# Kernel tuning notes

Measured on AMD Instinct MI355X. Metric: run time of the kernel, lower is better.

The kernel has to match this reference:

```python
import jax, jax.numpy as jnp
import numpy as np

DIM = 256
BETA = 4
B, L, L1 = 16, 2048, 4096
EPS = 1e-6


def setup_inputs() -> dict:
    key = jax.random.key(0)
    ks = jax.random.split(key, 20)
    d, db = DIM, DIM // BETA
    s = lambda *sh: 0.02
    inp = {
        "features": jax.random.normal(ks[0], (B, L, d), jnp.float32),
        "quires_box": jax.random.uniform(ks[1], (B, L1, 2), jnp.float32),
        "quires_features": jax.random.normal(ks[2], (B, L1, d), jnp.float32),
        "pos_feature": jax.random.normal(ks[3], (B, L1, d), jnp.float32),
        # contrast1 params
        "c1_w1": jax.random.normal(ks[4], (db, d), jnp.float32) * 0.02,
        "c1_b1": jnp.zeros((db,), jnp.float32),
        "c1_w2": jax.random.normal(ks[5], (d, db), jnp.float32) * 0.02,
        "c1_b2": jnp.zeros((d,), jnp.float32),
        "c1_g": jnp.ones((d,), jnp.float32),
        "c1_be": jnp.zeros((d,), jnp.float32),
        # contrast2 params
        "c2_w1": jax.random.normal(ks[6], (db, d), jnp.float32) * 0.02,
        "c2_b1": jnp.zeros((db,), jnp.float32),
        "c2_w2": jax.random.normal(ks[7], (d, db), jnp.float32) * 0.02,
        "c2_b2": jnp.zeros((d,), jnp.float32),
        "c2_g": jnp.ones((d,), jnp.float32),
        "c2_be": jnp.zeros((d,), jnp.float32),
        # gate MLP (Prediction: Linear(2d->d)+ReLU+Linear(d->2), dropout=identity at eval)
        "g_w1": jax.random.normal(ks[8], (d, 2 * d), jnp.float32) * 0.02,
        "g_b1": jnp.zeros((d,), jnp.float32),
        "g_w2": jax.random.normal(ks[9], (2, d), jnp.float32) * 0.02,
        "g_b2": jnp.zeros((2,), jnp.float32),
    }
    return inp


def _contrast(v1, v2, w1, b1, w2, b2, g, be):
    # v1, v2: [B, N, C]. Pointwise conv1 -> ReLU -> conv2 -> LayerNorm -> sigmoid -> *v1
    v = v1 * v2
    h = jax.nn.relu(jnp.einsum('bnc,dc->bnd', v, w1) + b1)  # [B,N,C/beta]
    u = jnp.einsum('bnd,cd->bnc', h, w2) + b2               # [B,N,C]
    mu = jnp.mean(u, axis=-1, keepdims=True)
    var = jnp.mean(jnp.square(u - mu), axis=-1, keepdims=True)
    ln = (u - mu) * jax.lax.rsqrt(var + EPS) * g + be
    return jax.nn.sigmoid(ln) * v1


def reference(features, quires_box, quires_features, pos_feature,
              c1_w1, c1_b1, c1_w2, c1_b2, c1_g, c1_be,
              c2_w1, c2_b1, c2_w2, c2_b2, c2_g, c2_be,
              g_w1, g_b1, g_w2, g_b2):
    Lf = features.shape[1]
    cx, w = quires_box[..., 0], quires_box[..., 1]
    roi_start = jnp.round(jnp.clip((cx - w / 2) * Lf, 0, Lf - 1)).astype(jnp.int32)
    roi_end = jnp.round(jnp.clip((cx + w / 2) * Lf, 0, Lf - 1)).astype(jnp.int32)
    sf = jnp.take_along_axis(features, roi_start[..., None], axis=1)  # [B,L1,C]
    ef = jnp.take_along_axis(features, roi_end[..., None], axis=1)    # [B,L1,C]
    sf = _contrast(sf, pos_feature, c1_w1, c1_b1, c1_w2, c1_b2, c1_g, c1_be)
    ef = _contrast(ef, pos_feature, c2_w1, c2_b1, c2_w2, c2_b2, c2_g, c2_be)
    pooled = (sf + ef) * 0.5  # aligned_len=True -> mean over the 2 boundaries
    x = jnp.concatenate([pooled, quires_features], axis=-1)  # [B,L1,2C]
    h = jax.nn.relu(jnp.einsum('bnc,dc->bnd', x, g_w1) + g_b1)
    gate = jax.nn.softmax(jnp.einsum('bnd,od->bno', h, g_w2) + g_b2, axis=-1)
    out = pooled * gate[..., 0:1] + quires_features * gate[..., 1:2]
    return jnp.swapaxes(out, 0, 1)  # [L1, B, C]
```

## Files before the change

kernel.cpp:

```cpp
#include <hip/hip_runtime.h>
#include <hip/hip_bf16.h>
#include <math.h>

typedef __attribute__((ext_vector_type(8))) short bf16x8;
typedef __attribute__((ext_vector_type(4))) float f32x4;
typedef __attribute__((ext_vector_type(2))) __fp16 f16x2;
typedef __attribute__((ext_vector_type(4))) unsigned int u32x4;
typedef __attribute__((ext_vector_type(2))) unsigned int u32x2;

constexpr int NB = 16, NQ = 4096, LF = 2048, C = 256;

__device__ __forceinline__ unsigned short bfbits(float x) {
    return __builtin_bit_cast(unsigned short, __float2bfloat16(x));
}
__device__ __forceinline__ unsigned pk2(float a, float b) {
    return (unsigned)bfbits(a) | ((unsigned)bfbits(b) << 16);
}
__device__ __forceinline__ float bflo(unsigned d) { return __builtin_bit_cast(float, d << 16); }
__device__ __forceinline__ float bfhi(unsigned d) { return __builtin_bit_cast(float, d & 0xffff0000u); }

__global__ void prep_weights(const float* __restrict__ c1w1, const float* __restrict__ c2w1,
                             const float* __restrict__ c1w2, const float* __restrict__ c2w2,
                             const float* __restrict__ gw1, unsigned short* __restrict__ ws)
{
    int t = blockIdx.x * 256 + threadIdx.x;
    const float* src; int K, nks, dstoff, f;
    if (t < 2048)      { src = c1w1; K = 256; nks = 8;  dstoff = 0;      f = t; }
    else if (t < 4096) { src = c2w1; K = 256; nks = 8;  dstoff = 16384;  f = t - 2048; }
    else if (t < 6144) { src = c1w2; K = 64;  nks = 2;  dstoff = 32768;  f = t - 4096; }
    else if (t < 8192) { src = c2w2; K = 64;  nks = 2;  dstoff = 49152;  f = t - 6144; }
    else               { src = gw1;  K = 512; nks = 16; dstoff = 65536;  f = t - 8192; }
    int l = f & 63, s = f >> 6;
    int nt = s / nks, ks = s % nks;
    int n  = nt * 16 + (l & 15);
    int k0 = ks * 32 + (l >> 4) * 8;
    unsigned short* d = ws + dstoff + (size_t)f * 8;
    const float* sp = src + (size_t)n * K + k0;
    #pragma unroll
    for (int e = 0; e < 8; ++e) d[e] = bfbits(sp[e]);
}

__device__ __forceinline__ void stage_chunk(const unsigned short* wsb, int chunk,
                                            unsigned short* dst, int wid, int l)
{
    const char* g = (const char*)wsb + (size_t)chunk * 32768 + wid * 1024 + (size_t)l * 16;
    char* d = (char*)dst + wid * 1024;
    #pragma unroll
    for (int i = 0; i < 16; ++i) {
        __builtin_amdgcn_global_load_lds(
            (const __attribute__((address_space(1))) void*)(g + i * 2048),
            (__attribute__((address_space(3))) void*)(d + i * 2048),
            16, 0, 0);
    }
}

__global__ __launch_bounds__(128, 2)
void semalign_v7(const float* __restrict__ feat,  const float* __restrict__ qbox,
                 const float* __restrict__ qfeat, const float* __restrict__ posf,
                 const float* __restrict__ c1b1,  const float* __restrict__ c1b2,
                 const float* __restrict__ c1g,   const float* __restrict__ c1be,
                 const float* __restrict__ c2b1,  const float* __restrict__ c2b2,
                 const float* __restrict__ c2g,   const float* __restrict__ c2be,
                 const float* __restrict__ gb1,   const float* __restrict__ gw2,
                 const float* __restrict__ gb2,
                 const unsigned short* __restrict__ wsb,
                 float* __restrict__ out)
{
    __shared__ __align__(16) unsigned short sW[2][16384];
    __shared__ __align__(16) unsigned short sP[2][16][256];

    const int tid = threadIdx.x, l = tid & 63, wid = tid >> 6;
    const int lr = l & 15, lg = l >> 4;
    const int rowb = blockIdx.x * 32 + wid * 16;
    const int q = rowb >> 4;
    const int b = lr;
    const int swz = (lr & 7) << 4;

    stage_chunk(wsb, 0, sW[0], wid, l);
    stage_chunk(wsb, 1, sW[1], wid, l);

    const float* prow = posf  + ((size_t)b * NQ + q) * C;
    const float* qrow = qfeat + ((size_t)b * NQ + q) * C;
    float cx = qbox[((size_t)b * NQ + q) * 2 + 0];
    float w  = qbox[((size_t)b * NQ + q) * 2 + 1];
    float fs = fminf(fmaxf((cx - 0.5f * w) * (float)LF, 0.f), (float)(LF - 1));
    float fe = fminf(fmaxf((cx + 0.5f * w) * (float)LF, 0.f), (float)(LF - 1));
    const float* srow = feat + ((size_t)b * LF + (int)rintf(fs)) * C;
    const float* erow = feat + ((size_t)b * LF + (int)rintf(fe)) * C;

    bf16x8 v1f[8], v2f[8];
    #pragma unroll
    for (int ks = 0; ks < 8; ++ks) {
        int k0 = ks * 32 + lg * 8;
        float4 s0 = *(const float4*)(srow + k0), s1 = *(const float4*)(srow + k0 + 4);
        float4 e0 = *(const float4*)(erow + k0), e1 = *(const float4*)(erow + k0 + 4);
        float4 p0 = *(const float4*)(prow + k0), p1 = *(const float4*)(prow + k0 + 4);
        u32x4 a, c;
        a[0] = pk2(s0.x * p0.x, s0.y * p0.y); a[1] = pk2(s0.z * p0.z, s0.w * p0.w);
        a[2] = pk2(s1.x * p1.x, s1.y * p1.y); a[3] = pk2(s1.z * p1.z, s1.w * p1.w);
        c[0] = pk2(e0.x * p0.x, e0.y * p0.y); c[1] = pk2(e0.z * p0.z, e0.w * p0.w);
        c[2] = pk2(e1.x * p1.x, e1.y * p1.y); c[3] = pk2(e1.z * p1.z, e1.w * p1.w);
        v1f[ks] = __builtin_bit_cast(bf16x8, a);
        v2f[ks] = __builtin_bit_cast(bf16x8, c);
    }

    __syncthreads();

    f32x4 a1[4] = {};
    {
        const char* wb = (const char*)sW[0];
        #pragma unroll
        for (int ks = 0; ks < 8; ++ks)
            #pragma unroll
            for (int nt = 0; nt < 4; ++nt) {
                bf16x8 wA = *(const bf16x8*)(wb + (nt * 8 + ks) * 1024 + l * 16);
                a1[nt] = __builtin_amdgcn_mfma_f32_16x16x32_bf16(wA, v1f[ks], a1[nt], 0, 0, 0);
            }
    }
    __syncthreads();
    stage_chunk(wsb, 2, sW[0], wid, l);

    char* hb = (char*)&sP[wid][0][0];
    bf16x8 hA0, hA1, hB0, hB1;
    {
        const char* wb = (const char*)sW[1];
        f32x4 a2[4] = {};
        #pragma unroll
        for (int ks = 0; ks < 8; ++ks)
            #pragma unroll
            for (int nt = 0; nt < 4; ++nt) {
                bf16x8 wB = *(const bf16x8*)(wb + (nt * 8 + ks) * 1024 + l * 16);
                a2[nt] = __builtin_amdgcn_mfma_f32_16x16x32_bf16(wB, v2f[ks], a2[nt], 0, 0, 0);
            }
        #pragma unroll
        for (int nt = 0; nt < 4; ++nt) {
            float4 b1v = *(const float4*)(c1b1 + nt * 16 + lg * 4);
            float4 b2v = *(const float4*)(c2b1 + nt * 16 + lg * 4);
            u32x2 wv;
            wv[0] = pk2(fmaxf(a1[nt][0] + b1v.x, 0.f), fmaxf(a1[nt][1] + b1v.y, 0.f));
            wv[1] = pk2(fmaxf(a1[nt][2] + b1v.z, 0.f), fmaxf(a1[nt][3] + b1v.w, 0.f));
            *(u32x2*)(hb + lr * 128 + ((nt * 32 + lg * 8) ^ swz)) = wv;
            wv[0] = pk2(fmaxf(a2[nt][0] + b2v.x, 0.f), fmaxf(a2[nt][1] + b2v.y, 0.f));
            wv[1] = pk2(fmaxf(a2[nt][2] + b2v.z, 0.f), fmaxf(a2[nt][3] + b2v.w, 0.f));
            *(u32x2*)(hb + 2048 + lr * 128 + ((nt * 32 + lg * 8) ^ swz)) = wv;
        }
        asm volatile("s_waitcnt lgkmcnt(0)" ::: "memory");
        hA0 = *(const bf16x8*)(hb + lr * 128 + ((0  + lg * 16) ^ swz));
        hA1 = *(const bf16x8*)(hb + lr * 128 + ((64 + lg * 16) ^ swz));
        hB0 = *(const bf16x8*)(hb + 2048 + lr * 128 + ((0  + lg * 16) ^ swz));
        hB1 = *(const bf16x8*)(hb + 2048 + lr * 128 + ((64 + lg * 16) ^ swz));
    }
    __syncthreads();
    stage_chunk(wsb, 3, sW[1], wid, l);

    f16x2 Ph[16][2];
    {
        const char* wb = (const char*)sW[0];
        f32x4 u0[16] = {};
        #pragma unroll
        for (int nt = 0; nt < 16; ++nt) {
            bf16x8 wA0 = *(const bf16x8*)(wb + (nt * 2 + 0) * 1024 + l * 16);
            bf16x8 wA1 = *(const bf16x8*)(wb + (nt * 2 + 1) * 1024 + l * 16);
            u0[nt] = __builtin_amdgcn_mfma_f32_16x16x32_bf16(wA0, hA0, u0[nt], 0, 0, 0);
            u0[nt] = __builtin_amdgcn_mfma_f32_16x16x32_bf16(wA1, hA1, u0[nt], 0, 0, 0);
        }
        float S = 0.f, Q2 = 0.f;
        #pragma unroll
        for (int nt = 0; nt < 16; ++nt) {
            float4 bv = *(const float4*)(c1b2 + nt * 16 + lg * 4);
            u0[nt][0] += bv.x; u0[nt][1] += bv.y; u0[nt][2] += bv.z; u0[nt][3] += bv.w;
            S  += u0[nt][0] + u0[nt][1] + u0[nt][2] + u0[nt][3];
            Q2 += u0[nt][0] * u0[nt][0] + u0[nt][1] * u0[nt][1]
                + u0[nt][2] * u0[nt][2] + u0[nt][3] * u0[nt][3];
        }
        S  += __shfl_xor(S, 16);  S  += __shfl_xor(S, 32);
        Q2 += __shfl_xor(Q2, 16); Q2 += __shfl_xor(Q2, 32);
        float mu  = S * (1.f / 256.f);
        float rsg = rsqrtf(Q2 * (1.f / 256.f) - mu * mu + 1e-6f);
        #pragma unroll
        for (int nt = 0; nt < 16; ++nt) {
            float4 gv  = *(const float4*)(c1g  + nt * 16 + lg * 4);
            float4 bev = *(const float4*)(c1be + nt * 16 + lg * 4);
            float4 xv  = *(const float4*)(srow + nt * 16 + lg * 4);
            float g4[4] = { gv.x, gv.y, gv.z, gv.w };
            float e4[4] = { bev.x, bev.y, bev.z, bev.w };
            float x4[4] = { xv.x, xv.y, xv.z, xv.w };
            float tm[4];
            #pragma unroll
            for (int r = 0; r < 4; ++r) {
                float ln = (u0[nt][r] - mu) * rsg * g4[r] + e4[r];
                float sg = 1.f / (1.f + __expf(-ln));
                tm[r] = 0.5f * sg * x4[r];
            }
            Ph[nt][0] = __builtin_amdgcn_cvt_pkrtz(tm[0], tm[1]);
            Ph[nt][1] = __builtin_amdgcn_cvt_pkrtz(tm[2], tm[3]);
        }
    }
    __syncthreads();
    stage_chunk(wsb, 4, sW[0], wid, l);

    bf16x8 qff[8];
    {
        const char* wb = (const char*)sW[1];
        f32x4 u1[16] = {};
        #pragma unroll
        for (int nt = 0; nt < 16; ++nt) {
            bf16x8 wB0 = *(const bf16x8*)(wb + (nt * 2 + 0) * 1024 + l * 16);
            bf16x8 wB1 = *(const bf16x8*)(wb + (nt * 2 + 1) * 1024 + l * 16);
            u1[nt] = __builtin_amdgcn_mfma_f32_16x16x32_bf16(wB0, hB0, u1[nt], 0, 0, 0);
            u1[nt] = __builtin_amdgcn_mfma_f32_16x16x32_bf16(wB1, hB1, u1[nt], 0, 0, 0);
        }
        float S = 0.f, Q2 = 0.f;
        #pragma unroll
        for (int nt = 0; nt < 16; ++nt) {
            float4 bv = *(const float4*)(c2b2 + nt * 16 + lg * 4);
            u1[nt][0] += bv.x; u1[nt][1] += bv.y; u1[nt][2] += bv.z; u1[nt][3] += bv.w;
            S  += u1[nt][0] + u1[nt][1] + u1[nt][2] + u1[nt][3];
            Q2 += u1[nt][0] * u1[nt][0] + u1[nt][1] * u1[nt][1]
                + u1[nt][2] * u1[nt][2] + u1[nt][3] * u1[nt][3];
        }
        S  += __shfl_xor(S, 16);  S  += __shfl_xor(S, 32);
        Q2 += __shfl_xor(Q2, 16); Q2 += __shfl_xor(Q2, 32);
        float mu  = S * (1.f / 256.f);
        float rsg = rsqrtf(Q2 * (1.f / 256.f) - mu * mu + 1e-6f);
        #pragma unroll
        for (int nt = 0; nt < 16; ++nt) {
            float4 gv  = *(const float4*)(c2g  + nt * 16 + lg * 4);
            float4 bev = *(const float4*)(c2be + nt * 16 + lg * 4);
            float4 xv  = *(const float4*)(erow + nt * 16 + lg * 4);
            float g4[4] = { gv.x, gv.y, gv.z, gv.w };
            float e4[4] = { bev.x, bev.y, bev.z, bev.w };
            float x4[4] = { xv.x, xv.y, xv.z, xv.w };
            float pm[4];
            #pragma unroll
            for (int r = 0; r < 4; ++r) {
                float ln = (u1[nt][r] - mu) * rsg * g4[r] + e4[r];
                float sg = 1.f / (1.f + __expf(-ln));
                pm[r] = (float)Ph[nt][r >> 1][r & 1] + 0.5f * sg * x4[r];
            }
            u32x2 wv;
            wv[0] = pk2(pm[0], pm[1]); wv[1] = pk2(pm[2], pm[3]);
            *(u32x2*)(hb + lr * 512 + ((nt * 32 + lg * 8) ^ swz)) = wv;
        }
        #pragma unroll
        for (int ks = 0; ks < 8; ++ks) {
            int k0 = ks * 32 + lg * 8;
            float4 q0v = *(const float4*)(qrow + k0), q1v = *(const float4*)(qrow + k0 + 4);
            u32x4 a;
            a[0] = pk2(q0v.x, q0v.y); a[1] = pk2(q0v.z, q0v.w);
            a[2] = pk2(q1v.x, q1v.y); a[3] = pk2(q1v.z, q1v.w);
            qff[ks] = __builtin_bit_cast(bf16x8, a);
        }
        asm volatile("s_waitcnt lgkmcnt(0)" ::: "memory");
    }
    bf16x8 xfp[8];
    #pragma unroll
    for (int ks = 0; ks < 8; ++ks)
        xfp[ks] = *(const bf16x8*)(hb + lr * 512 + ((ks * 64 + lg * 16) ^ swz));
    __syncthreads();
    stage_chunk(wsb, 5, sW[1], wid, l);

    float t0 = 0.f, t1 = 0.f;
    #pragma unroll
    for (int cc = 0; cc < 8; ++cc) {
        const char* wb = (const char*)sW[cc & 1];
        f32x4 ga0 = {}, ga1 = {};
        #pragma unroll
        for (int kk = 0; kk < 16; ++kk) {
            bf16x8 xk = (kk < 8) ? xfp[kk] : qff[kk - 8];
            bf16x8 wA = *(const bf16x8*)(wb + kk * 1024 + l * 16);
            bf16x8 wB = *(const bf16x8*)(wb + (16 + kk) * 1024 + l * 16);
            ga0 = __builtin_amdgcn_mfma_f32_16x16x32_bf16(wA, xk, ga0, 0, 0, 0);
            ga1 = __builtin_amdgcn_mfma_f32_16x16x32_bf16(wB, xk, ga1, 0, 0, 0);
        }
        #pragma unroll
        for (int t2 = 0; t2 < 2; ++t2) {
            f32x4 ga = t2 ? ga1 : ga0;
            int nt = cc * 2 + t2;
            float4 gbv = *(const float4*)(gb1 + nt * 16 + lg * 4);
            float4 w0v = *(const float4*)(gw2 + nt * 16 + lg * 4);
            float4 w1v = *(const float4*)(gw2 + 256 + nt * 16 + lg * 4);
            float gb4[4] = { gbv.x, gbv.y, gbv.z, gbv.w };
            float w04[4] = { w0v.x, w0v.y, w0v.z, w0v.w };
            float w14[4] = { w1v.x, w1v.y, w1v.z, w1v.w };
            #pragma unroll
            for (int r = 0; r < 4; ++r) {
                float hv = fmaxf(ga[r] + gb4[r], 0.f);
                t0 += hv * w04[r]; t1 += hv * w14[r];
            }
        }
        __syncthreads();
        if (cc < 6) stage_chunk(wsb, 6 + cc, sW[cc & 1], wid, l);
    }

    t0 += __shfl_xor(t0, 16); t0 += __shfl_xor(t0, 32);
    t1 += __shfl_xor(t1, 16); t1 += __shfl_xor(t1, 32);
    float g0 = 1.f / (1.f + __expf((t1 + gb2[1]) - (t0 + gb2[0])));
    float g1v = 1.f - g0;

    float* orow = out + (size_t)(rowb + lr) * C;
    #pragma unroll
    for (int ks = 0; ks < 8; ++ks) {
        u32x4 pu = __builtin_bit_cast(u32x4, xfp[ks]);
        u32x4 qu = __builtin_bit_cast(u32x4, qff[ks]);
        float4 o0, o1;
        o0.x = bflo(pu[0]) * g0 + bflo(qu[0]) * g1v;
        o0.y = bfhi(pu[0]) * g0 + bfhi(qu[0]) * g1v;
        o0.z = bflo(pu[1]) * g0 + bflo(qu[1]) * g1v;
        o0.w = bfhi(pu[1]) * g0 + bfhi(qu[1]) * g1v;
        o1.x = bflo(pu[2]) * g0 + bflo(qu[2]) * g1v;
        o1.y = bfhi(pu[2]) * g0 + bfhi(qu[2]) * g1v;
        o1.z = bflo(pu[3]) * g0 + bflo(qu[3]) * g1v;
        o1.w = bfhi(pu[3]) * g0 + bfhi(qu[3]) * g1v;
        *(float4*)(orow + ks * 32 + lg * 8)     = o0;
        *(float4*)(orow + ks * 32 + lg * 8 + 4) = o1;
    }
}

extern "C" void kernel_launch(void* const* d_in, const int* in_sizes, int n_in,
                              void* d_out, int out_size, void* d_ws, size_t ws_size,
                              hipStream_t stream) {
    const float* feat  = (const float*)d_in[0];
    const float* qbox  = (const float*)d_in[1];
    const float* qfeat = (const float*)d_in[2];
    const float* posf  = (const float*)d_in[3];
    const float* c1w1  = (const float*)d_in[4];
    const float* c1b1  = (const float*)d_in[5];
    const float* c1w2  = (const float*)d_in[6];
    const float* c1b2  = (const float*)d_in[7];
    const float* c1g   = (const float*)d_in[8];
    const float* c1be  = (const float*)d_in[9];
    const float* c2w1  = (const float*)d_in[10];
    const float* c2b1  = (const float*)d_in[11];
    const float* c2w2  = (const float*)d_in[12];
    const float* c2b2  = (const float*)d_in[13];
    const float* c2g   = (const float*)d_in[14];
    const float* c2be  = (const float*)d_in[15];
    const float* gw1   = (const float*)d_in[16];
    const float* gb1   = (const float*)d_in[17];
    const float* gw2   = (const float*)d_in[18];
    const float* gb2   = (const float*)d_in[19];
    float* out = (float*)d_out;
    unsigned short* wsb = (unsigned short*)d_ws;

    prep_weights<<<96, 256, 0, stream>>>(c1w1, c2w1, c1w2, c2w2, gw1, wsb);

    dim3 grid((NB * NQ) / 32), block(128);
    semalign_v7<<<grid, block, 0, stream>>>(
        feat, qbox, qfeat, posf,
        c1b1, c1b2, c1g, c1be,
        c2b1, c2b2, c2g, c2be,
        gb1, gw2, gb2, wsb, out);
}
```

Measured before the change: 182.9 us.

## Stream weights through LDS in 8KB sub-chunks to shrink shared memory footprint

Weight staging is split from 32KB chunks into 8KB sub-chunks, so the double buffer drops from 64KB to 16KB of LDS. Every GEMM phase (contrast conv1 and conv2 for both branches, and the gate MLP) is restructured to consume one sub-chunk, sync, then prefetch the sub-chunk two ahead. The aim is lower LDS use per block, so more blocks can be resident per CU and hide gather latency. The cost is several times more barriers and smaller prefetch units, which leaves less load-compute overlap per step.

```diff
diff --git a/kernel.cpp b/kernel.cpp
--- a/kernel.cpp
+++ b/kernel.cpp
@@ -40,13 +40,13 @@
     for (int e = 0; e < 8; ++e) d[e] = bfbits(sp[e]);
 }
 
-__device__ __forceinline__ void stage_chunk(const unsigned short* wsb, int chunk,
-                                            unsigned short* dst, int wid, int l)
+__device__ __forceinline__ void stage_sub(const unsigned short* wsb, int sub,
+                                          unsigned short* dst, int wid, int l)
 {
-    const char* g = (const char*)wsb + (size_t)chunk * 32768 + wid * 1024 + (size_t)l * 16;
+    const char* g = (const char*)wsb + (size_t)sub * 8192 + (size_t)wid * 1024 + (size_t)l * 16;
     char* d = (char*)dst + wid * 1024;
     #pragma unroll
-    for (int i = 0; i < 16; ++i) {
+    for (int i = 0; i < 4; ++i) {
         __builtin_amdgcn_global_load_lds(
             (const __attribute__((address_space(1))) void*)(g + i * 2048),
             (__attribute__((address_space(3))) void*)(d + i * 2048),
@@ -55,18 +55,18 @@
 }
 
 __global__ __launch_bounds__(128, 2)
-void semalign_v7(const float* __restrict__ feat,  const float* __restrict__ qbox,
-                 const float* __restrict__ qfeat, const float* __restrict__ posf,
-                 const float* __restrict__ c1b1,  const float* __restrict__ c1b2,
-                 const float* __restrict__ c1g,   const float* __restrict__ c1be,
-                 const float* __restrict__ c2b1,  const float* __restrict__ c2b2,
-                 const float* __restrict__ c2g,   const float* __restrict__ c2be,
-                 const float* __restrict__ gb1,   const float* __restrict__ gw2,
-                 const float* __restrict__ gb2,
-                 const unsigned short* __restrict__ wsb,
-                 float* __restrict__ out)
+void semalign_v10(const float* __restrict__ feat,  const float* __restrict__ qbox,
+                  const float* __restrict__ qfeat, const float* __restrict__ posf,
+                  const float* __restrict__ c1b1,  const float* __restrict__ c1b2,
+                  const float* __restrict__ c1g,   const float* __restrict__ c1be,
+                  const float* __restrict__ c2b1,  const float* __restrict__ c2b2,
+                  const float* __restrict__ c2g,   const float* __restrict__ c2be,
+                  const float* __restrict__ gb1,   const float* __restrict__ gw2,
+                  const float* __restrict__ gb2,
+                  const unsigned short* __restrict__ wsb,
+                  float* __restrict__ out)
 {
-    __shared__ __align__(16) unsigned short sW[2][16384];
+    __shared__ __align__(16) unsigned short sW[2][4096];
     __shared__ __align__(16) unsigned short sP[2][16][256];
 
     const int tid = threadIdx.x, l = tid & 63, wid = tid >> 6;
@@ -76,8 +76,8 @@
     const int b = lr;
     const int swz = (lr & 7) << 4;
 
-    stage_chunk(wsb, 0, sW[0], wid, l);
-    stage_chunk(wsb, 1, sW[1], wid, l);
+    stage_sub(wsb, 0, sW[0], wid, l);
+    stage_sub(wsb, 1, sW[1], wid, l);
 
     const float* prow = posf  + ((size_t)b * NQ + q) * C;
     const float* qrow = qfeat + ((size_t)b * NQ + q) * C;
@@ -106,32 +106,24 @@
 
     __syncthreads();
 
-    f32x4 a1[4] = {};
-    {
-        const char* wb = (const char*)sW[0];
-        #pragma unroll
-        for (int ks = 0; ks < 8; ++ks)
-            #pragma unroll
-            for (int nt = 0; nt < 4; ++nt) {
-                bf16x8 wA = *(const bf16x8*)(wb + (nt * 8 + ks) * 1024 + l * 16);
-                a1[nt] = __builtin_amdgcn_mfma_f32_16x16x32_bf16(wA, v1f[ks], a1[nt], 0, 0, 0);
-            }
-    }
-    __syncthreads();
-    stage_chunk(wsb, 2, sW[0], wid, l);
+    f32x4 a1[4] = {}, a2[4] = {};
+    #pragma unroll
+    for (int ss = 0; ss < 8; ++ss) {
+        const char* wb = (const char*)sW[ss & 1];
+        int nt = ss & 3;
+        #pragma unroll
+        for (int ks = 0; ks < 8; ++ks) {
+            bf16x8 wf = *(const bf16x8*)(wb + ks * 1024 + l * 16);
+            if (ss < 4) a1[nt] = __builtin_amdgcn_mfma_f32_16x16x32_bf16(wf, v1f[ks], a1[nt], 0, 0, 0);
+            else        a2[nt] = __builtin_amdgcn_mfma_f32_16x16x32_bf16(wf, v2f[ks], a2[nt], 0, 0, 0);
+        }
+        __syncthreads();
+        stage_sub(wsb, ss + 2, sW[ss & 1], wid, l);
+    }
 
     char* hb = (char*)&sP[wid][0][0];
     bf16x8 hA0, hA1, hB0, hB1;
     {
-        const char* wb = (const char*)sW[1];
-        f32x4 a2[4] = {};
-        #pragma unroll
-        for (int ks = 0; ks < 8; ++ks)
-            #pragma unroll
-            for (int nt = 0; nt < 4; ++nt) {
-                bf16x8 wB = *(const bf16x8*)(wb + (nt * 8 + ks) * 1024 + l * 16);
-                a2[nt] = __builtin_amdgcn_mfma_f32_16x16x32_bf16(wB, v2f[ks], a2[nt], 0, 0, 0);
-            }
         #pragma unroll
         for (int nt = 0; nt < 4; ++nt) {
             float4 b1v = *(const float4*)(c1b1 + nt * 16 + lg * 4);
@@ -150,19 +142,23 @@
         hB0 = *(const bf16x8*)(hb + 2048 + lr * 128 + ((0  + lg * 16) ^ swz));
         hB1 = *(const bf16x8*)(hb + 2048 + lr * 128 + ((64 + lg * 16) ^ swz));
     }
-    __syncthreads();
-    stage_chunk(wsb, 3, sW[1], wid, l);
 
     f16x2 Ph[16][2];
     {
-        const char* wb = (const char*)sW[0];
         f32x4 u0[16] = {};
         #pragma unroll
-        for (int nt = 0; nt < 16; ++nt) {
-            bf16x8 wA0 = *(const bf16x8*)(wb + (nt * 2 + 0) * 1024 + l * 16);
-            bf16x8 wA1 = *(const bf16x8*)(wb + (nt * 2 + 1) * 1024 + l * 16);
-            u0[nt] = __builtin_amdgcn_mfma_f32_16x16x32_bf16(wA0, hA0, u0[nt], 0, 0, 0);
-            u0[nt] = __builtin_amdgcn_mfma_f32_16x16x32_bf16(wA1, hA1, u0[nt], 0, 0, 0);
+        for (int ss = 0; ss < 4; ++ss) {
+            const char* wb = (const char*)sW[ss & 1];
+            #pragma unroll
+            for (int i = 0; i < 4; ++i) {
+                int nt = ss * 4 + i;
+                bf16x8 w0 = *(const bf16x8*)(wb + (i * 2 + 0) * 1024 + l * 16);
+                bf16x8 w1 = *(const bf16x8*)(wb + (i * 2 + 1) * 1024 + l * 16);
+                u0[nt] = __builtin_amdgcn_mfma_f32_16x16x32_bf16(w0, hA0, u0[nt], 0, 0, 0);
+                u0[nt] = __builtin_amdgcn_mfma_f32_16x16x32_bf16(w1, hA1, u0[nt], 0, 0, 0);
+            }
+            __syncthreads();
+            stage_sub(wsb, 10 + ss, sW[ss & 1], wid, l);
         }
         float S = 0.f, Q2 = 0.f;
         #pragma unroll
@@ -196,19 +192,23 @@
             Ph[nt][1] = __builtin_amdgcn_cvt_pkrtz(tm[2], tm[3]);
         }
     }
-    __syncthreads();
-    stage_chunk(wsb, 4, sW[0], wid, l);
 
     bf16x8 qff[8];
     {
-        const char* wb = (const char*)sW[1];
         f32x4 u1[16] = {};
         #pragma unroll
-        for (int nt = 0; nt < 16; ++nt) {
-            bf16x8 wB0 = *(const bf16x8*)(wb + (nt * 2 + 0) * 1024 + l * 16);
-            bf16x8 wB1 = *(const bf16x8*)(wb + (nt * 2 + 1) * 1024 + l * 16);
-            u1[nt] = __builtin_amdgcn_mfma_f32_16x16x32_bf16(wB0, hB0, u1[nt], 0, 0, 0);
-            u1[nt] = __builtin_amdgcn_mfma_f32_16x16x32_bf16(wB1, hB1, u1[nt], 0, 0, 0);
+        for (int ss = 0; ss < 4; ++ss) {
+            const char* wb = (const char*)sW[ss & 1];
+            #pragma unroll
+            for (int i = 0; i < 4; ++i) {
+                int nt = ss * 4 + i;
+                bf16x8 w0 = *(const bf16x8*)(wb + (i * 2 + 0) * 1024 + l * 16);
+                bf16x8 w1 = *(const bf16x8*)(wb + (i * 2 + 1) * 1024 + l * 16);
+                u1[nt] = __builtin_amdgcn_mfma_f32_16x16x32_bf16(w0, hB0, u1[nt], 0, 0, 0);
+                u1[nt] = __builtin_amdgcn_mfma_f32_16x16x32_bf16(w1, hB1, u1[nt], 0, 0, 0);
+            }
+            __syncthreads();
+            stage_sub(wsb, 14 + ss, sW[ss & 1], wid, l);
         }
         float S = 0.f, Q2 = 0.f;
         #pragma unroll
@@ -257,40 +257,35 @@
     #pragma unroll
     for (int ks = 0; ks < 8; ++ks)
         xfp[ks] = *(const bf16x8*)(hb + lr * 512 + ((ks * 64 + lg * 16) ^ swz));
-    __syncthreads();
-    stage_chunk(wsb, 5, sW[1], wid, l);
 
     float t0 = 0.f, t1 = 0.f;
     #pragma unroll
-    for (int cc = 0; cc < 8; ++cc) {
-        const char* wb = (const char*)sW[cc & 1];
-        f32x4 ga0 = {}, ga1 = {};
-        #pragma unroll
-        for (int kk = 0; kk < 16; ++kk) {
-            bf16x8 xk = (kk < 8) ? xfp[kk] : qff[kk - 8];
-            bf16x8 wA = *(const bf16x8*)(wb + kk * 1024 + l * 16);
-            bf16x8 wB = *(const bf16x8*)(wb + (16 + kk) * 1024 + l * 16);
-            ga0 = __builtin_amdgcn_mfma_f32_16x16x32_bf16(wA, xk, ga0, 0, 0, 0);
-            ga1 = __builtin_amdgcn_mfma_f32_16x16x32_bf16(wB, xk, ga1, 0, 0, 0);
-        }
-        #pragma unroll
-        for (int t2 = 0; t2 < 2; ++t2) {
-            f32x4 ga = t2 ? ga1 : ga0;
-            int nt = cc * 2 + t2;
-            float4 gbv = *(const float4*)(gb1 + nt * 16 + lg * 4);
-            float4 w0v = *(const float4*)(gw2 + nt * 16 + lg * 4);
-            float4 w1v = *(const float4*)(gw2 + 256 + nt * 16 + lg * 4);
-            float gb4[4] = { gbv.x, gbv.y, gbv.z, gbv.w };
-            float w04[4] = { w0v.x, w0v.y, w0v.z, w0v.w };
-            float w14[4] = { w1v.x, w1v.y, w1v.z, w1v.w };
-            #pragma unroll
-            for (int r = 0; r < 4; ++r) {
-                float hv = fmaxf(ga[r] + gb4[r], 0.f);
-                t0 += hv * w04[r]; t1 += hv * w14[r];
-            }
-        }
-        __syncthreads();
-        if (cc < 6) stage_chunk(wsb, 6 + cc, sW[cc & 1], wid, l);
+    for (int nt = 0; nt < 16; ++nt) {
+        f32x4 ga = {};
+        #pragma unroll
+        for (int half = 0; half < 2; ++half) {
+            int s = 16 + nt * 2 + half;
+            const char* wb = (const char*)sW[s & 1];
+            #pragma unroll
+            for (int j = 0; j < 8; ++j) {
+                bf16x8 xk = half ? qff[j] : xfp[j];
+                bf16x8 wf = *(const bf16x8*)(wb + j * 1024 + l * 16);
+                ga = __builtin_amdgcn_mfma_f32_16x16x32_bf16(wf, xk, ga, 0, 0, 0);
+            }
+            __syncthreads();
+            if (s + 2 < 48) stage_sub(wsb, s + 2, sW[s & 1], wid, l);
+        }
+        float4 gbv = *(const float4*)(gb1 + nt * 16 + lg * 4);
+        float4 w0v = *(const float4*)(gw2 + nt * 16 + lg * 4);
+        float4 w1v = *(const float4*)(gw2 + 256 + nt * 16 + lg * 4);
+        float gb4[4] = { gbv.x, gbv.y, gbv.z, gbv.w };
+        float w04[4] = { w0v.x, w0v.y, w0v.z, w0v.w };
+        float w14[4] = { w1v.x, w1v.y, w1v.z, w1v.w };
+        #pragma unroll
+        for (int r = 0; r < 4; ++r) {
+            float hv = fmaxf(ga[r] + gb4[r], 0.f);
+            t0 += hv * w04[r]; t1 += hv * w14[r];
+        }
     }
 
     t0 += __shfl_xor(t0, 16); t0 += __shfl_xor(t0, 32);
@@ -346,7 +341,7 @@
     prep_weights<<<96, 256, 0, stream>>>(c1w1, c2w1, c1w2, c2w2, gw1, wsb);
 
     dim3 grid((NB * NQ) / 32), block(128);
-    semalign_v7<<<grid, block, 0, stream>>>(
+    semalign_v10<<<grid, block, 0, stream>>>(
         feat, qbox, qfeat, posf,
         c1b1, c1b2, c1g, c1be,
         c2b1, c2b2, c2g, c2be,
```

New measurement: 317.7 us. 1.74x slower.
